# Optimization experiments

Hardware: AMD Instinct MI355X
Metric: run time of the kernel (lower is better)

The kernel has to match this reference:

```python
import jax, jax.numpy as jnp
import numpy as np

# ---- constants mirroring init_kwargs ----
S = 128          # sheet_units
KA = 25          # aff_cf_units
C = 2            # aff_cf_channels
KL = 25          # lat_cf_units
EXC = 9          # exc_units
DA = 1           # aff_cf_dilation
DL = 1           # lat_cf_dilation
HOMEO_TARGET = 0.04
STRENGTH = 1.0

# ---- radial helper masks (get_circle / get_radial_cos) ----
def _dist(n):
    g = jnp.arange(n, dtype=jnp.float32) - (n - 1) / 2.0
    return jnp.sqrt(g[:, None] ** 2 + g[None, :] ** 2)

def _circle(n, r):
    return (_dist(n) < r).astype(jnp.float32)

def _rcos(n, wl):
    return jnp.cos(_dist(n) * jnp.pi / wl)

# afferent envelope: [C*KA*KA], channel-major like torch repeat+view
_ae = _rcos(KA, KA) ** 2 * _circle(KA, KA / 2)
_ae = _ae / _ae.max()
AFF_ENV = jnp.tile(_ae.reshape(1, KA * KA), (C, 1)).reshape(C * KA * KA)

# lateral (LRI) envelope: [KL*KL]
_inh = _rcos(KL, EXC / DL) ** 2 * _circle(KL, EXC / (2 * DL))
_le = _rcos(KL, KL) ** 2 * (1.0 - _inh) * _circle(KL, KL / 2)
LRI_ENV = (_le / _le.max()).reshape(KL * KL)

def _unfold(x, k, dil):
    """x: [C,H,W] -> patches [L, C*k*k], torch F.unfold ordering (C slowest)."""
    Cc, H, W = x.shape
    out = H - dil * (k - 1)
    idx = jnp.arange(out)[:, None] + dil * jnp.arange(k)[None, :]  # [out,k]
    p = x[:, idx, :]          # [C,out,k,W]
    p = p[:, :, :, idx]       # [C,out,k,out,k]
    p = p.transpose(1, 3, 0, 2, 4)  # [out_i,out_j,C,ki,kj]
    return p.reshape(out * out, Cc * k * k)

def setup_inputs() -> dict:
    key = jax.random.key(0)
    k1, k2 = jax.random.split(key)
    in_size = S + DA * (KA - 1)  # 152
    x = jax.random.uniform(k1, (1, C, in_size, in_size), dtype=jnp.float32)
    rfs = jax.random.uniform(k2, (S * S, C * KA * KA, 1), dtype=jnp.float32)
    rfs = rfs / rfs.sum(1, keepdims=True)
    lat_weights = jnp.ones((S * S, KL * KL, 1), jnp.float32) / (KL * KL)
    adathresh = jnp.zeros((1, 1, S, S), jnp.float32)
    return {"x": x, "rfs": rfs, "lat_weights": lat_weights, "adathresh": adathresh}

def _forward(x, rfs, lat_weights, adathresh):
    relu = jax.nn.relu
    rfs = relu(rfs)                 # no_grad positive clamp of params
    lw = relu(lat_weights)
    # afferent: unfold + envelope + per-pixel dot (bmm with [L,F,1])
    tiles = _unfold(x[0], KA, DA) * AFF_ENV[None, :]          # [L, C*KA*KA]
    raw_aff = jnp.einsum('lf,lf->l', tiles, rfs[:, :, 0]).reshape(S, S)
    aff = jax.lax.stop_gradient(raw_aff) - adathresh[0, 0]
    lat = relu(aff)
    # lateral inhibition: pad so unfold yields S*S positions
    p = DL * (KL - 1) // 2
    lt = _unfold(jnp.pad(lat, p)[None], KL, DL) * LRI_ENV[None, :]  # [L, KL*KL]
    lat_neg = jnp.einsum('lf,lf->l', lt, jax.lax.stop_gradient(lw)[:, :, 0]).reshape(S, S)
    lat = lat - lat_neg
    lat = jnp.tanh(relu(lat * STRENGTH + aff))
    # hebbian lateral correlations term (learning_flag path)
    lt2 = _unfold(jnp.pad(lat, p, constant_values=HOMEO_TARGET)[None], KL, DL) * LRI_ENV[None, :]
    weighted = lt2 * lat.reshape(S * S, 1)
    lat_correlations = jnp.einsum('lf,lf->', weighted, lw[:, :, 0])
    return (raw_aff.reshape(1, 1, S, S), lat.reshape(1, 1, S, S),
            lat_correlations, tiles[:, None, :])

def reference(x, rfs, lat_weights, adathresh):
    return _forward(x, rfs, lat_weights, adathresh)
```

## Files before the change

kernel.cpp:

```cpp
#include <hip/hip_runtime.h>
#include <math.h>

#define S 128
#define KA 25
#define PATCH 625
#define FEAT 1250
#define PI_F 3.14159265358979323846f
#define PADW 152
#define PADA (PADW * PADW)

#define WS_LRI 0
#define WS_AE 640
#define WS_LAT0P 1280
#define WS_LATFP 24384
#define WS_PART 47488
#define WS_AEL 48512
#define NPART 1024

__device__ __forceinline__ int div25(int r) { return (r * 10486) >> 18; }
__device__ __forceinline__ int eslot(int r) { return (r & 3) * 160 + (r >> 2); }

__device__ __forceinline__ void gld16(const float* g, float* l) {
    __builtin_amdgcn_global_load_lds(
        (const __attribute__((address_space(1))) void*)g,
        (__attribute__((address_space(3))) void*)l, 16, 0, 0);
}
#define VMCNT(N) asm volatile("s_waitcnt vmcnt(" #N ")" ::: "memory"); \
                 __builtin_amdgcn_sched_barrier(0)

__global__ __launch_bounds__(256) void k_init(float* __restrict__ ws) {
    const int tid = threadIdx.x;
    if (blockIdx.x == 0) {
        __shared__ float s_tmp[640];
        __shared__ float s_red[4];
        float m = 0.0f;
        for (int r = tid; r < PATCH; r += 256) {
            int qi = div25(r);
            float di = (float)qi - 12.0f;
            float dj = (float)(r - 25 * qi) - 12.0f;
            float d = sqrtf(di * di + dj * dj);
            float ae = 0.0f, le = 0.0f;
            if (d < 12.5f) {
                float c1 = cosf(d * (PI_F / 25.0f));
                ae = c1 * c1;
                float inh = 0.0f;
                if (d < 4.5f) {
                    float c2 = cosf(d * (PI_F / 9.0f));
                    inh = c2 * c2;
                }
                le = c1 * c1 * (1.0f - inh);
            }
            ws[WS_AE + eslot(r)] = ae;
            ws[WS_AEL + r] = ae;
            s_tmp[r] = le;
            m = fmaxf(m, le);
        }
        for (int o = 32; o; o >>= 1) m = fmaxf(m, __shfl_down(m, o));
        if (!(tid & 63)) s_red[tid >> 6] = m;
        __syncthreads();
        float inv = 1.0f / fmaxf(fmaxf(s_red[0], s_red[1]),
                                 fmaxf(s_red[2], s_red[3]));
        for (int r = tid; r < PATCH; r += 256) ws[WS_LRI + r] = s_tmp[r] * inv;
    }
    const int gid = blockIdx.x * 256 + tid;
    const int gsz = gridDim.x * 256;
    for (int i = gid; i < 2 * PADA; i += gsz) {
        if (i < PADA) ws[WS_LAT0P + i] = 0.0f;
        else          ws[WS_LATFP + i - PADA] = 0.04f;
    }
}

__global__ __launch_bounds__(256) void k_aff(const float* __restrict__ x,
                                             const float* __restrict__ rfs,
                                             const float* __restrict__ ada,
                                             float* __restrict__ raw_aff,
                                             float* __restrict__ ws) {
    __shared__ float s_ae[640];
    __shared__ float s_x[2][25][28];
    const int tid = threadIdx.x, lane = tid & 63, wv = tid >> 6;
    const int blk = blockIdx.x;
    const int li = blk >> 5;
    const int lj0 = (blk & 31) << 2;

    for (int i = tid; i < 640; i += 256) s_ae[i] = ws[WS_AE + i];
    for (int i = tid; i < 1400; i += 256) {
        int c = i >= 700;
        int rm = i - c * 700;
        int ki = rm / 28;
        int col = rm - ki * 28;
        s_x[c][ki][(col & 3) * 7 + (col >> 2)] =
            x[c * PADA + (li + ki) * PADW + lj0 + col];
    }
    __syncthreads();

    const int tc = wv;
    const int l = li * 128 + lj0 + tc;
    const long B = (long)l * FEAT;
    const int peel = (l & 1) ? 2 : 0;

    float acc = 0.0f;
    if (lane < peel) {
        int f = lane;
        int col = f + tc;
        acc += s_x[0][0][(col & 3) * 7 + (col >> 2)] * s_ae[eslot(f)]
               * fmaxf(rfs[B + f], 0.0f);
    }

    const float* __restrict__ rb = rfs + B + peel;
    const float4 rv0 = *reinterpret_cast<const float4*>(rb + 4 * lane);
    const float4 rv1 = *reinterpret_cast<const float4*>(rb + 4 * (lane + 64));
    const float4 rv2 = *reinterpret_cast<const float4*>(rb + 4 * (lane + 128));
    const float4 rv3 = *reinterpret_cast<const float4*>(rb + 4 * (lane + 192));
    float4 rv4 = {0.0f, 0.0f, 0.0f, 0.0f};
    if (lane < 56) rv4 = *reinterpret_cast<const float4*>(rb + 4 * (lane + 256));

    auto consume = [&](const float4& rv, int k) {
        const int f0 = peel + 4 * k;
#pragma unroll
        for (int j = 0; j < 4; ++j) {
            int f = f0 + j;
            int c = (f >= PATCH) ? 1 : 0;
            int r = f - c * PATCH;
            int ki = div25(r);
            int col = r - 25 * ki + tc;
            float t = s_x[c][ki][(col & 3) * 7 + (col >> 2)] * s_ae[eslot(r)];
            acc += t * fmaxf((&rv.x)[j], 0.0f);
        }
    };
    consume(rv0, lane);
    consume(rv1, lane + 64);
    consume(rv2, lane + 128);
    consume(rv3, lane + 192);
    if (lane < 56) consume(rv4, lane + 256);

    if (lane < 2 - peel) {
        int f = 1248 + lane;
        int r = f - PATCH;
        int ki = div25(r);
        int col = r - 25 * ki + tc;
        acc += s_x[1][ki][(col & 3) * 7 + (col >> 2)] * s_ae[eslot(r)]
               * fmaxf(rfs[B + f], 0.0f);
    }

    for (int o = 32; o; o >>= 1) acc += __shfl_down(acc, o);
    if (!lane) {
        raw_aff[l] = acc;
        ws[WS_LAT0P + (li + 12) * PADW + (lj0 + tc + 12)] =
            fmaxf(acc - ada[l], 0.0f);
    }
}

__device__ __forceinline__ void tiles_epilogue(
        const float* __restrict__ x, float* __restrict__ tiles,
        const float* __restrict__ ws, float* e_ae, float* e_x,
        int cc, int li, int lj0, int tc0, int lane, int tid) {
    for (int i = tid; i < 625; i += 256) e_ae[i] = ws[WS_AEL + i];
    for (int i = tid; i < 1000; i += 256) {
        int ki = i / 40, col = i - ki * 40;
        e_x[i] = x[cc * PADA + (li + ki) * PADW + lj0 + col];
    }
    __syncthreads();
#pragma unroll
    for (int n = 0; n < 4; ++n) {
        const int tc = tc0 + n;
        const long B = (long)(li * 128 + lj0 + tc) * FEAT + cc * PATCH;
#pragma unroll
        for (int j = 0; j < 10; ++j) {
            int r = j * 64 + lane;
            if (j < 9 || lane < 49) {
                int ki = div25(r), kj = r - 25 * ki;
                tiles[B + r] = e_x[ki * 40 + kj + tc] * e_ae[r];
            }
        }
    }
}

__global__ __launch_bounds__(256) void k_lat(const float* __restrict__ raw_aff,
                                             const float* __restrict__ ada,
                                             const float* __restrict__ lw,
                                             const float* __restrict__ x,
                                             float* __restrict__ latf,
                                             float* __restrict__ tiles,
                                             float* __restrict__ ws) {
    __shared__ float s_le[640];
    __shared__ float s_g[25][40];
    __shared__ float s_st[4][2][640];
    const int tid = threadIdx.x, lane = tid & 63, wv = tid >> 6;
    const int blk = blockIdx.x;
    const int li = blk >> 3;
    const int lj0 = (blk & 7) << 4;

    for (int i = tid; i < 625; i += 256) s_le[i] = ws[WS_LRI + i];
    for (int i = tid; i < 1000; i += 256) {
        int ki = i / 40;
        int col = i - ki * 40;
        s_g[ki][col] = ws[WS_LAT0P + (li + ki) * PADW + lj0 + col];
    }
    __syncthreads();

    const int tc0 = wv << 2;
    const int l0 = li * 128 + lj0 + tc0;

    float acc_ht[4], ra[4], ad[4];
#define HT(n) { \
        const int l = l0 + (n); const long B = (long)l * PATCH; \
        const int peel = (4 - (l & 3)) & 3; \
        const int fmax4 = (PATCH - peel) & ~3; \
        const int tcnt = (PATCH - peel) & 3; \
        float a = 0.0f; \
        if (lane < peel) { \
            int f = lane; int ki = div25(f); int kj = f - 25 * ki; \
            a += s_g[ki][kj + tc0 + (n)] * s_le[f] * fmaxf(lw[B + f], 0.0f); \
        } \
        if (lane < tcnt) { \
            int f = peel + fmax4 + lane; int ki = div25(f); int kj = f - 25 * ki; \
            a += s_g[ki][kj + tc0 + (n)] * s_le[f] * fmaxf(lw[B + f], 0.0f); \
        } \
        if (!lane) { ra[n] = raw_aff[l]; ad[n] = ada[l]; } \
        acc_ht[n] = a; }
    HT(0) HT(1) HT(2) HT(3)
#undef HT

    auto stage = [&](int n, float* buf) {
        const int l = l0 + n;
        const long B = (long)l * PATCH;
        const int peel = (4 - (l & 3)) & 3;
        const int rem = ((PATCH - peel) >> 2) - 128;
        const float* gp = lw + B + peel + 4 * lane;
        gld16(gp,       buf);
        gld16(gp + 256, buf + 256);
        if (lane < rem) gld16(gp + 512, buf + 512);
    };
    auto consume = [&](int n, const float* buf, float accin, float rav,
                       float adv) {
        const int l = l0 + n;
        const int peel = (4 - (l & 3)) & 3;
        const int fmax4 = (PATCH - peel) & ~3;
        const int tc = tc0 + n;
        float acc = accin;
#pragma unroll
        for (int j = 0; j < 10; ++j) {
            int fh = j * 64 + lane;
            if (j < 9 || fh < fmax4) {
                float wval = buf[fh];
                int f = peel + fh;
                int ki = div25(f);
                int kj = f - 25 * ki;
                acc += s_g[ki][kj + tc] * s_le[f] * fmaxf(wval, 0.0f);
            }
        }
        for (int o = 32; o; o >>= 1) acc += __shfl_down(acc, o);
        if (!lane) {
            float aff_l = rav - adv;
            float lat0_l = fmaxf(aff_l, 0.0f);
            float v = (lat0_l - acc)  + aff_l;
            float lv = tanhf(fmaxf(v, 0.0f));
            latf[l] = lv;
            ws[WS_LATFP + (li + 12) * PADW + lj0 + tc + 12] = lv;
        }
    };

    float* buf0 = &s_st[wv][0][0];
    float* buf1 = &s_st[wv][1][0];
    __builtin_amdgcn_sched_barrier(0);
    stage(0, buf0);
    stage(1, buf1);
    VMCNT(3);
    consume(0, buf0, acc_ht[0], ra[0], ad[0]);
    stage(2, buf0);
    VMCNT(5);
    consume(1, buf1, acc_ht[1], ra[1], ad[1]);
    stage(3, buf1);
    VMCNT(5);
    consume(2, buf0, acc_ht[2], ra[2], ad[2]);
    VMCNT(2);
    consume(3, buf1, acc_ht[3], ra[3], ad[3]);

    __syncthreads();
    tiles_epilogue(x, tiles, ws, &s_st[0][0][0], &s_st[1][0][0],
                   0, li, lj0, tc0, lane, tid);
}

__global__ __launch_bounds__(256) void k_corr(const float* __restrict__ latf,
                                              const float* __restrict__ lw,
                                              const float* __restrict__ x,
                                              float* __restrict__ tiles,
                                              float* __restrict__ ws) {
    __shared__ float s_le[640];
    __shared__ float s_g[25][40];
    __shared__ float s_st[4][2][640];
    __shared__ float s_red[4];
    const int tid = threadIdx.x, lane = tid & 63, wv = tid >> 6;
    const int blk = blockIdx.x;
    const int li = blk >> 3;
    const int lj0 = (blk & 7) << 4;

    for (int i = tid; i < 625; i += 256) s_le[i] = ws[WS_LRI + i];
    for (int i = tid; i < 1000; i += 256) {
        int ki = i / 40;
        int col = i - ki * 40;
        s_g[ki][col] = ws[WS_LATFP + (li + ki) * PADW + lj0 + col];
    }
    __syncthreads();

    const int tc0 = wv << 2;
    const int l0 = li * 128 + lj0 + tc0;

    float acc_ht[4], lf[4];
#define HT(n) { \
        const int l = l0 + (n); const long B = (long)l * PATCH; \
        const int peel = (4 - (l & 3)) & 3; \
        const int fmax4 = (PATCH - peel) & ~3; \
        const int tcnt = (PATCH - peel) & 3; \
        float a = 0.0f; \
        if (lane < peel) { \
            int f = lane; int ki = div25(f); int kj = f - 25 * ki; \
            a += s_g[ki][kj + tc0 + (n)] * s_le[f] * fmaxf(lw[B + f], 0.0f); \
        } \
        if (lane < tcnt) { \
            int f = peel + fmax4 + lane; int ki = div25(f); int kj = f - 25 * ki; \
            a += s_g[ki][kj + tc0 + (n)] * s_le[f] * fmaxf(lw[B + f], 0.0f); \
        } \
        if (!lane) lf[n] = latf[l]; \
        acc_ht[n] = a; }
    HT(0) HT(1) HT(2) HT(3)
#undef HT

    auto stage = [&](int n, float* buf) {
        const int l = l0 + n;
        const long B = (long)l * PATCH;
        const int peel = (4 - (l & 3)) & 3;
        const int rem = ((PATCH - peel) >> 2) - 128;
        const float* gp = lw + B + peel + 4 * lane;
        gld16(gp,       buf);
        gld16(gp + 256, buf + 256);
        if (lane < rem) gld16(gp + 512, buf + 512);
    };
    float wsum = 0.0f;
    auto consume = [&](int n, const float* buf, float accin, float lfv) {
        const int l = l0 + n;
        const int peel = (4 - (l & 3)) & 3;
        const int fmax4 = (PATCH - peel) & ~3;
        const int tc = tc0 + n;
        float acc = accin;
#pragma unroll
        for (int j = 0; j < 10; ++j) {
            int fh = j * 64 + lane;
            if (j < 9 || fh < fmax4) {
                float wval = buf[fh];
                int f = peel + fh;
                int ki = div25(f);
                int kj = f - 25 * ki;
                acc += s_g[ki][kj + tc] * s_le[f] * fmaxf(wval, 0.0f);
            }
        }
        for (int o = 32; o; o >>= 1) acc += __shfl_down(acc, o);
        if (!lane) wsum += acc * lfv;
    };

    float* buf0 = &s_st[wv][0][0];
    float* buf1 = &s_st[wv][1][0];
    __builtin_amdgcn_sched_barrier(0);
    stage(0, buf0);
    stage(1, buf1);
    VMCNT(3);
    consume(0, buf0, acc_ht[0], lf[0]);
    stage(2, buf0);
    VMCNT(3);
    consume(1, buf1, acc_ht[1], lf[1]);
    stage(3, buf1);
    VMCNT(3);
    consume(2, buf0, acc_ht[2], lf[2]);
    VMCNT(0);
    consume(3, buf1, acc_ht[3], lf[3]);

    if (!lane) s_red[wv] = wsum;
    __syncthreads();
    if (!tid)
        ws[WS_PART + blk] = s_red[0] + s_red[1] + s_red[2] + s_red[3];

    __syncthreads();
    tiles_epilogue(x, tiles, ws, &s_st[0][0][0], &s_st[1][0][0],
                   1, li, lj0, tc0, lane, tid);
}

__global__ __launch_bounds__(256) void k_reduce(const float* __restrict__ ws,
                                                float* __restrict__ corr) {
    __shared__ float s_red[4];
    const int tid = threadIdx.x;
    const int lane = tid & 63, wv = tid >> 6;
    float acc = 0.0f;
    for (int i = tid; i < NPART; i += 256) acc += ws[WS_PART + i];
    for (int o = 32; o; o >>= 1) acc += __shfl_down(acc, o);
    if (!lane) s_red[wv] = acc;
    __syncthreads();
    if (!tid) corr[0] = s_red[0] + s_red[1] + s_red[2] + s_red[3];
}

extern "C" void kernel_launch(void* const* d_in, const int* in_sizes, int n_in,
                              void* d_out, int out_size, void* d_ws, size_t ws_size,
                              hipStream_t stream) {
    const float* x   = (const float*)d_in[0];
    const float* rfs = (const float*)d_in[1];
    const float* lw  = (const float*)d_in[2];
    const float* ada = (const float*)d_in[3];

    float* out      = (float*)d_out;
    float* raw_aff  = out;
    float* latf     = out + S * S;
    float* corr     = out + 2 * S * S;
    float* tiles    = out + 2 * S * S + 1;
    float* ws       = (float*)d_ws;

    k_init<<<16, 256, 0, stream>>>(ws);
    k_aff<<<4096, 256, 0, stream>>>(x, rfs, ada, raw_aff, ws);
    k_lat<<<1024, 256, 0, stream>>>(raw_aff, ada, lw, x, latf, tiles, ws);
    k_corr<<<1024, 256, 0, stream>>>(latf, lw, x, tiles, ws);
    k_reduce<<<1, 256, 0, stream>>>(ws, corr);
}
```

Baseline: 215.6 us.

## Drop init and reduce kernels by recomputing envelopes and last-block reduction

Removes the k_init and k_reduce launches. Envelope tables are now recomputed per block in shared memory, pad borders are zeroed and the 0.04 buffer is filled inside k_aff, and the final correlation sum is done by the last k_corr block using an atomic ticket counter. This saves two kernel launches and their gaps. In exchange every block does redundant sqrt/cos work, and the border init in k_aff races benignly with the interior writes. The design also relies on the atomic-counter pattern being ordered correctly.

Result: slower. 295.4 us (+37.0%).

```diff
diff --git a/kernel.cpp b/kernel.cpp
--- a/kernel.cpp
+++ b/kernel.cpp
@@ -9,16 +9,44 @@
 #define PADW 152
 #define PADA (PADW * PADW)
 
-#define WS_LRI 0
-#define WS_AE 640
-#define WS_LAT0P 1280
-#define WS_LATFP 24384
-#define WS_PART 47488
-#define WS_AEL 48512
+#define WS_LAT0P 0
+#define WS_LATFP 23168
+#define WS_PART 46336
+#define WS_CTR 47360
 #define NPART 1024
 
 __device__ __forceinline__ int div25(int r) { return (r * 10486) >> 18; }
 __device__ __forceinline__ int eslot(int r) { return (r & 3) * 160 + (r >> 2); }
+
+__device__ __forceinline__ float aff_env(int r) {
+    int qi = div25(r);
+    float di = (float)qi - 12.0f;
+    float dj = (float)(r - 25 * qi) - 12.0f;
+    float d = sqrtf(di * di + dj * dj);
+    float ae = 0.0f;
+    if (d < 12.5f) {
+        float c1 = cosf(d * (PI_F / 25.0f));
+        ae = c1 * c1;
+    }
+    return ae;
+}
+__device__ __forceinline__ float lri_env(int r) {
+    int qi = div25(r);
+    float di = (float)qi - 12.0f;
+    float dj = (float)(r - 25 * qi) - 12.0f;
+    float d = sqrtf(di * di + dj * dj);
+    float le = 0.0f;
+    if (d < 12.5f) {
+        float c1 = cosf(d * (PI_F / 25.0f));
+        float inh = 0.0f;
+        if (d < 4.5f) {
+            float c2 = cosf(d * (PI_F / 9.0f));
+            inh = c2 * c2;
+        }
+        le = c1 * c1 * (1.0f - inh);
+    }
+    return le;
+}
 
 __device__ __forceinline__ void gld16(const float* g, float* l) {
     __builtin_amdgcn_global_load_lds(
@@ -27,48 +55,6 @@
 }
 #define VMCNT(N) asm volatile("s_waitcnt vmcnt(" #N ")" ::: "memory"); \
                  __builtin_amdgcn_sched_barrier(0)
-
-__global__ __launch_bounds__(256) void k_init(float* __restrict__ ws) {
-    const int tid = threadIdx.x;
-    if (blockIdx.x == 0) {
-        __shared__ float s_tmp[640];
-        __shared__ float s_red[4];
-        float m = 0.0f;
-        for (int r = tid; r < PATCH; r += 256) {
-            int qi = div25(r);
-            float di = (float)qi - 12.0f;
-            float dj = (float)(r - 25 * qi) - 12.0f;
-            float d = sqrtf(di * di + dj * dj);
-            float ae = 0.0f, le = 0.0f;
-            if (d < 12.5f) {
-                float c1 = cosf(d * (PI_F / 25.0f));
-                ae = c1 * c1;
-                float inh = 0.0f;
-                if (d < 4.5f) {
-                    float c2 = cosf(d * (PI_F / 9.0f));
-                    inh = c2 * c2;
-                }
-                le = c1 * c1 * (1.0f - inh);
-            }
-            ws[WS_AE + eslot(r)] = ae;
-            ws[WS_AEL + r] = ae;
-            s_tmp[r] = le;
-            m = fmaxf(m, le);
-        }
-        for (int o = 32; o; o >>= 1) m = fmaxf(m, __shfl_down(m, o));
-        if (!(tid & 63)) s_red[tid >> 6] = m;
-        __syncthreads();
-        float inv = 1.0f / fmaxf(fmaxf(s_red[0], s_red[1]),
-                                 fmaxf(s_red[2], s_red[3]));
-        for (int r = tid; r < PATCH; r += 256) ws[WS_LRI + r] = s_tmp[r] * inv;
-    }
-    const int gid = blockIdx.x * 256 + tid;
-    const int gsz = gridDim.x * 256;
-    for (int i = gid; i < 2 * PADA; i += gsz) {
-        if (i < PADA) ws[WS_LAT0P + i] = 0.0f;
-        else          ws[WS_LATFP + i - PADA] = 0.04f;
-    }
-}
 
 __global__ __launch_bounds__(256) void k_aff(const float* __restrict__ x,
                                              const float* __restrict__ rfs,
@@ -82,7 +68,7 @@
     const int li = blk >> 5;
     const int lj0 = (blk & 31) << 2;
 
-    for (int i = tid; i < 640; i += 256) s_ae[i] = ws[WS_AE + i];
+    for (int r = tid; r < PATCH; r += 256) s_ae[eslot(r)] = aff_env(r);
     for (int i = tid; i < 1400; i += 256) {
         int c = i >= 700;
         int rm = i - c * 700;
@@ -90,6 +76,19 @@
         int col = rm - ki * 28;
         s_x[c][ki][(col & 3) * 7 + (col >> 2)] =
             x[c * PADA + (li + ki) * PADW + lj0 + col];
+    }
+    {
+        const int gid = blk * 256 + tid;
+        if (gid < 2 * PADA) {
+            if (gid < PADA) {
+                int pi = gid / PADW, pj = gid - pi * PADW;
+                if (pi < 12 || pi >= 140 || pj < 12 || pj >= 140)
+                    ws[WS_LAT0P + gid] = 0.0f;
+            } else {
+                ws[WS_LATFP + gid - PADA] = 0.04f;
+            }
+        }
+        if (gid == 0) *(unsigned*)(ws + WS_CTR) = 0u;
     }
     __syncthreads();
 
@@ -152,9 +151,9 @@
 
 __device__ __forceinline__ void tiles_epilogue(
         const float* __restrict__ x, float* __restrict__ tiles,
-        const float* __restrict__ ws, float* e_ae, float* e_x,
+        float* e_ae, float* e_x,
         int cc, int li, int lj0, int tc0, int lane, int tid) {
-    for (int i = tid; i < 625; i += 256) e_ae[i] = ws[WS_AEL + i];
+    for (int r = tid; r < PATCH; r += 256) e_ae[r] = aff_env(r);
     for (int i = tid; i < 1000; i += 256) {
         int ki = i / 40, col = i - ki * 40;
         e_x[i] = x[cc * PADA + (li + ki) * PADW + lj0 + col];
@@ -185,16 +184,30 @@
     __shared__ float s_le[640];
     __shared__ float s_g[25][40];
     __shared__ float s_st[4][2][640];
+    __shared__ float s_red[4];
     const int tid = threadIdx.x, lane = tid & 63, wv = tid >> 6;
     const int blk = blockIdx.x;
     const int li = blk >> 3;
     const int lj0 = (blk & 7) << 4;
 
-    for (int i = tid; i < 625; i += 256) s_le[i] = ws[WS_LRI + i];
+    float m = 0.0f;
+    for (int r = tid; r < PATCH; r += 256) {
+        float le = lri_env(r);
+        s_le[r] = le;
+        m = fmaxf(m, le);
+    }
     for (int i = tid; i < 1000; i += 256) {
         int ki = i / 40;
         int col = i - ki * 40;
         s_g[ki][col] = ws[WS_LAT0P + (li + ki) * PADW + lj0 + col];
+    }
+    for (int o = 32; o; o >>= 1) m = fmaxf(m, __shfl_down(m, o));
+    if (!lane) s_red[wv] = m;
+    __syncthreads();
+    {
+        float inv = 1.0f / fmaxf(fmaxf(s_red[0], s_red[1]),
+                                 fmaxf(s_red[2], s_red[3]));
+        for (int r = tid; r < PATCH; r += 256) s_le[r] *= inv;
     }
     __syncthreads();
 
@@ -277,7 +290,7 @@
     consume(3, buf1, acc_ht[3], ra[3], ad[3]);
 
     __syncthreads();
-    tiles_epilogue(x, tiles, ws, &s_st[0][0][0], &s_st[1][0][0],
+    tiles_epilogue(x, tiles, &s_st[0][0][0], &s_st[1][0][0],
                    0, li, lj0, tc0, lane, tid);
 }
 
@@ -285,21 +298,36 @@
                                               const float* __restrict__ lw,
                                               const float* __restrict__ x,
                                               float* __restrict__ tiles,
+                                              float* __restrict__ corr,
                                               float* __restrict__ ws) {
     __shared__ float s_le[640];
     __shared__ float s_g[25][40];
     __shared__ float s_st[4][2][640];
     __shared__ float s_red[4];
+    __shared__ int s_last;
     const int tid = threadIdx.x, lane = tid & 63, wv = tid >> 6;
     const int blk = blockIdx.x;
     const int li = blk >> 3;
     const int lj0 = (blk & 7) << 4;
 
-    for (int i = tid; i < 625; i += 256) s_le[i] = ws[WS_LRI + i];
+    float m = 0.0f;
+    for (int r = tid; r < PATCH; r += 256) {
+        float le = lri_env(r);
+        s_le[r] = le;
+        m = fmaxf(m, le);
+    }
     for (int i = tid; i < 1000; i += 256) {
         int ki = i / 40;
         int col = i - ki * 40;
         s_g[ki][col] = ws[WS_LATFP + (li + ki) * PADW + lj0 + col];
+    }
+    for (int o = 32; o; o >>= 1) m = fmaxf(m, __shfl_down(m, o));
+    if (!lane) s_red[wv] = m;
+    __syncthreads();
+    {
+        float inv = 1.0f / fmaxf(fmaxf(s_red[0], s_red[1]),
+                                 fmaxf(s_red[2], s_red[3]));
+        for (int r = tid; r < PATCH; r += 256) s_le[r] *= inv;
     }
     __syncthreads();
 
@@ -380,21 +408,27 @@
         ws[WS_PART + blk] = s_red[0] + s_red[1] + s_red[2] + s_red[3];
 
     __syncthreads();
-    tiles_epilogue(x, tiles, ws, &s_st[0][0][0], &s_st[1][0][0],
+    tiles_epilogue(x, tiles, &s_st[0][0][0], &s_st[1][0][0],
                    1, li, lj0, tc0, lane, tid);
-}
-
-__global__ __launch_bounds__(256) void k_reduce(const float* __restrict__ ws,
-                                                float* __restrict__ corr) {
-    __shared__ float s_red[4];
-    const int tid = threadIdx.x;
-    const int lane = tid & 63, wv = tid >> 6;
-    float acc = 0.0f;
-    for (int i = tid; i < NPART; i += 256) acc += ws[WS_PART + i];
-    for (int o = 32; o; o >>= 1) acc += __shfl_down(acc, o);
-    if (!lane) s_red[wv] = acc;
-    __syncthreads();
-    if (!tid) corr[0] = s_red[0] + s_red[1] + s_red[2] + s_red[3];
+
+    if (tid == 0) {
+        __threadfence();
+        unsigned old = __hip_atomic_fetch_add(
+            (unsigned*)(ws + WS_CTR), 1u,
+            __ATOMIC_ACQ_REL, __HIP_MEMORY_SCOPE_AGENT);
+        s_last = (old == (unsigned)(NPART - 1));
+    }
+    __syncthreads();
+    if (s_last) {
+        float a = 0.0f;
+        for (int i = tid; i < NPART; i += 256)
+            a += __hip_atomic_load(ws + WS_PART + i,
+                                   __ATOMIC_RELAXED, __HIP_MEMORY_SCOPE_AGENT);
+        for (int o = 32; o; o >>= 1) a += __shfl_down(a, o);
+        if (!lane) s_red[wv] = a;
+        __syncthreads();
+        if (!tid) corr[0] = s_red[0] + s_red[1] + s_red[2] + s_red[3];
+    }
 }
 
 extern "C" void kernel_launch(void* const* d_in, const int* in_sizes, int n_in,
@@ -412,9 +446,7 @@
     float* tiles    = out + 2 * S * S + 1;
     float* ws       = (float*)d_ws;
 
-    k_init<<<16, 256, 0, stream>>>(ws);
     k_aff<<<4096, 256, 0, stream>>>(x, rfs, ada, raw_aff, ws);
     k_lat<<<1024, 256, 0, stream>>>(raw_aff, ada, lw, x, latf, tiles, ws);
-    k_corr<<<1024, 256, 0, stream>>>(latf, lw, x, tiles, ws);
-    k_reduce<<<1, 256, 0, stream>>>(ws, corr);
-}
+    k_corr<<<1024, 256, 0, stream>>>(latf, lw, x, tiles, corr, ws);
+}
```
